# Optimization experiments

Measured on AMD Instinct MI355X. Metric: run time of the kernel, lower is better.

## Reference

```python
import jax, jax.numpy as jnp
import numpy as np

B, T, DM, H, DQ, FF, L, OUT = 4, 512, 768, 8, 32, 3072, 6, 80
D_REL = 100   # relative_positional_distance
NEG = 1e8
LN_EPS = 1e-5


def _layer_norm(x, w, b):
    mu = jnp.mean(x, axis=-1, keepdims=True)
    var = jnp.mean((x - mu) ** 2, axis=-1, keepdims=True)
    return (x - mu) * jax.lax.rsqrt(var + LN_EPS) * w + b


def _attention(x, wq, wk, wv, wo, rel):
    # x: (B,T,DM); wq/wk/wv: (H,DM,DQ); wo: (H,DQ,DM); rel: (H, 2*D_REL-1, DQ)
    Tq = x.shape[1]
    q = jnp.einsum('btf,hfa->bhta', x, wq) / (DQ ** 0.5)   # q pre-scaled (as in source)
    k = jnp.einsum('btf,hfa->bhta', x, wk)
    v = jnp.einsum('btf,hfa->bhta', x, wv)
    logits = jnp.einsum('bhqa,bhka->bhqk', q, k)

    # relative positional logits over the 199 learned offsets
    rel_log = jnp.einsum('bhqd,hmd->bhqm', q, rel)          # (B,H,T,2*D_REL-1)
    pad = Tq - D_REL
    if pad > 0:
        # zero-pad to 2T-1 rel positions, then mask out-of-range offsets with -1e8
        rel_log = jnp.pad(rel_log, ((0, 0), (0, 0), (0, 0), (pad, pad)))
        m = jnp.arange(2 * Tq - 1)
        oob = (m < pad) | (m >= 2 * Tq - 1 - pad)
        rel_log = rel_log - NEG * oob.astype(rel_log.dtype)
    else:
        start = D_REL - Tq
        rel_log = rel_log[..., start:start + 2 * Tq - 1]
    # relative -> absolute indexing: pos[..., i, j] = rel_log[..., i, (j - i) + T - 1]
    idx = jnp.arange(Tq)[None, :] - jnp.arange(Tq)[:, None] + (Tq - 1)   # (T,T)
    pos = jnp.take_along_axis(rel_log, idx[None, None], axis=-1)         # (B,H,T,T)

    probs = jax.nn.softmax(logits + pos, axis=-1)
    o = jnp.einsum('bhqk,bhka->bhqa', probs, v)
    return jnp.einsum('bhta,had->btd', o, wo)


def _forward(x, wq, wk, wv, wo, rel, lin1_w, lin1_b, lin2_w, lin2_b,
             ln1_w, ln1_b, ln2_w, ln2_b, w_out, b_out):
    def step(h, p):
        (q, k, v, o, r, l1w, l1b, l2w, l2b, n1w, n1b, n2w, n2b) = p
        a = _attention(h, q, k, v, o, r)
        h = _layer_norm(h + a, n1w, n1b)                  # post-norm, residual
        ff = jnp.maximum(h @ l1w.T + l1b, 0.0) @ l2w.T + l2b
        h = _layer_norm(h + ff, n2w, n2b)
        return h, None
    h, _ = jax.lax.scan(step, x, (wq, wk, wv, wo, rel, lin1_w, lin1_b,
                                  lin2_w, lin2_b, ln1_w, ln1_b, ln2_w, ln2_b))
    return h @ w_out.T + b_out                            # (B,T,OUT)


def setup_inputs() -> dict:
    key = jax.random.key(0)
    ks = jax.random.split(key, 16)
    n = lambda k, shape, scale: (jax.random.normal(k, shape, dtype=jnp.float32) * scale)
    s_qkv = (2.0 / (DM + DQ)) ** 0.5      # xavier_normal_ scale
    s_o = (2.0 / (DQ + DM)) ** 0.5
    return {
        'x':      n(ks[0], (B, T, DM), 1.0),
        'wq':     n(ks[1], (L, H, DM, DQ), s_qkv),
        'wk':     n(ks[2], (L, H, DM, DQ), s_qkv),
        'wv':     n(ks[3], (L, H, DM, DQ), s_qkv),
        'wo':     n(ks[4], (L, H, DQ, DM), s_o),
        'rel':    n(ks[5], (L, H, 2 * D_REL - 1, DQ), DQ ** -0.5),
        'lin1_w': n(ks[6], (L, FF, DM), DM ** -0.5),
        'lin1_b': jnp.zeros((L, FF), jnp.float32),
        'lin2_w': n(ks[7], (L, DM, FF), FF ** -0.5),
        'lin2_b': jnp.zeros((L, DM), jnp.float32),
        'ln1_w':  jnp.ones((L, DM), jnp.float32),
        'ln1_b':  jnp.zeros((L, DM), jnp.float32),
        'ln2_w':  jnp.ones((L, DM), jnp.float32),
        'ln2_b':  jnp.zeros((L, DM), jnp.float32),
        'w_out':  n(ks[8], (OUT, DM), DM ** -0.5),
        'b_out':  jnp.zeros((OUT,), jnp.float32),
    }


def reference(x, wq, wk, wv, wo, rel, lin1_w, lin1_b, lin2_w, lin2_b,
              ln1_w, ln1_b, ln2_w, ln2_b, w_out, b_out):
    return _forward(x, wq, wk, wv, wo, rel, lin1_w, lin1_b, lin2_w, lin2_b,
                    ln1_w, ln1_b, ln2_w, ln2_b, w_out, b_out)
```

## Files before the change

kernel.cpp:

```cpp
#include <hip/hip_runtime.h>

typedef _Float16 f16;
typedef f16 f16x8 __attribute__((ext_vector_type(8)));
typedef f16 f16x4 __attribute__((ext_vector_type(4)));
typedef float f32x4 __attribute__((ext_vector_type(4)));

#define B_ 4
#define T_ 512
#define DM_ 768
#define H_ 8
#define DQ_ 32
#define FF_ 3072
#define L_ 6
#define OUT_ 80
#define M_ (B_*T_)

__device__ __forceinline__ void gload16(const f16* g, f16* l) {
    __builtin_amdgcn_global_load_lds(
        (const __attribute__((address_space(1))) unsigned int*)g,
        (__attribute__((address_space(3))) unsigned int*)l, 16, 0, 0);
}

template<int N> __device__ __forceinline__ void wait_vm() {
    if constexpr (N == 0)      asm volatile("s_waitcnt vmcnt(0)" ::: "memory");
    else if constexpr (N == 3) asm volatile("s_waitcnt vmcnt(3)" ::: "memory");
    else if constexpr (N == 4) asm volatile("s_waitcnt vmcnt(4)" ::: "memory");
    else if constexpr (N == 6) asm volatile("s_waitcnt vmcnt(6)" ::: "memory");
    else if constexpr (N == 8) asm volatile("s_waitcnt vmcnt(8)" ::: "memory");
    else                       asm volatile("s_waitcnt vmcnt(0)" ::: "memory");
}


#define PKU_X  196608L
#define PKU_L1 (PKU_X + 1769472L)
#define PKU_L2 (PKU_L1 + 1769472L)
#define PKB_VEC 14592
#define PKB_LIN 1632
#define PKB_QKV 1728
#define PKB_WO  1152
#define PKB_TOTAL (PKB_VEC + PKB_LIN + PKB_QKV + PKB_WO)

__global__ void pack_all_kernel(
    const float* __restrict__ x, const float* __restrict__ wq, const float* __restrict__ wk,
    const float* __restrict__ wv, const float* __restrict__ wo, const float* __restrict__ rel,
    const float* __restrict__ lin1w, const float* __restrict__ lin2w, const float* __restrict__ wout,
    f16* __restrict__ xH, f16* __restrict__ BTqkv, f16* __restrict__ BTwo,
    f16* __restrict__ lin1H, f16* __restrict__ lin2H, f16* __restrict__ woutH, f16* __restrict__ relH)
{
    __shared__ float tile[64 * 33];
    const int bid = blockIdx.x, tid = threadIdx.x;
    if (bid < PKB_VEC) {
        const long u = (long)bid * 256 + tid;
        const float* src; f16* dst; long off;
        if (u < PKU_X)       { src = x;     dst = xH;    off = u; }
        else if (u < PKU_L1) { src = lin1w; dst = lin1H; off = u - PKU_X; }
        else                 { src = lin2w; dst = lin2H; off = u - PKU_L1; }
        const float4 v0 = ((const float4*)src)[off * 2];
        const float4 v1 = ((const float4*)src)[off * 2 + 1];
        f16x8 o;
        o[0] = (f16)v0.x; o[1] = (f16)v0.y; o[2] = (f16)v0.z; o[3] = (f16)v0.w;
        o[4] = (f16)v1.x; o[5] = (f16)v1.y; o[6] = (f16)v1.z; o[7] = (f16)v1.w;
        ((f16x8*)dst)[off] = o;
    } else if (bid < PKB_VEC + PKB_LIN) {
        const long u = (long)(bid - PKB_VEC) * 256 + tid;
        if (u < 98304) {
            const int k = (int)(u % 768), n = (int)(u / 768);
            woutH[u] = (n < OUT_) ? (f16)wout[n * 768 + k] : (f16)0;
        } else {
            const long v2 = u - 98304;
            const int a = (int)(v2 & 31);
            const long t = v2 >> 5;
            const int d = (int)(t % 208);
            const int lh = (int)(t / 208);
            relH[v2] = (d < 199) ? (f16)rel[((long)lh * 199 + d) * 32 + a] : (f16)0;
        }
    } else if (bid < PKB_VEC + PKB_LIN + PKB_QKV) {
        const int g = bid - (PKB_VEC + PKB_LIN);
        const int kb = g % 12;
        const int grp = g / 12;
        const int h = grp & 7, sec = (grp >> 3) % 3, l = grp / 24;
        const float* w = (sec == 0) ? wq : (sec == 1 ? wk : wv);
        const float* src = w + (((long)l * 8 + h) * 768 + kb * 64) * 32;
        const float scale = (sec == 0) ? 0.17677669529663687f : 1.f;
#pragma unroll
        for (int p = 0; p < 2; ++p) {
            const int kk = p * 32 + (tid >> 3), a = (tid & 7) * 4;
            const float4 v = *(const float4*)(src + (long)kk * 32 + a);
            tile[kk * 33 + a]     = v.x * scale;
            tile[kk * 33 + a + 1] = v.y * scale;
            tile[kk * 33 + a + 2] = v.z * scale;
            tile[kk * 33 + a + 3] = v.w * scale;
        }
        __syncthreads();
        f16* dst = BTqkv + ((long)l * 768 + sec * 256 + h * 32) * 768 + kb * 64;
        {
            const int a = tid >> 3, k8 = (tid & 7) * 8;
            f16x8 o;
#pragma unroll
            for (int e = 0; e < 8; ++e) o[e] = (f16)tile[(k8 + e) * 33 + a];
            *(f16x8*)(dst + (long)a * 768 + k8) = o;
        }
    } else {
        const int g = bid - (PKB_VEC + PKB_LIN + PKB_QKV);
        const int nb = g % 24;
        const int tmp = g / 24;
        const int kb2 = tmp % 8, l = tmp / 8;
        const float* src = wo + ((long)l * 256 + kb2 * 32) * 768 + nb * 32;
        {
            const int r = tid >> 3, c = (tid & 7) * 4;
            const float4 v = *(const float4*)(src + (long)r * 768 + c);
            tile[r * 33 + c]     = v.x;
            tile[r * 33 + c + 1] = v.y;
            tile[r * 33 + c + 2] = v.z;
            tile[r * 33 + c + 3] = v.w;
        }
        __syncthreads();
        if (tid < 128) {
            const int n = tid >> 2, k8 = (tid & 3) * 8;
            f16x8 o;
#pragma unroll
            for (int e = 0; e < 8; ++e) o[e] = (f16)tile[(k8 + e) * 33 + n];
            f16* dst = BTwo + ((long)l * 768 + nb * 32 + n) * 256 + kb2 * 32 + k8;
            *(f16x8*)dst = o;
        }
    }
}

__device__ __forceinline__ void xcd_tile(int BM, int BN, int& m0, int& n0) {
    const int gx = gridDim.x;
    const int id = blockIdx.y * gx + blockIdx.x;
    const int cpx = (gx * gridDim.y) >> 3;
    const int t = (id & 7) * cpx + (id >> 3);
    m0 = (t / gx) * BM;
    n0 = (t % gx) * BN;
}


template<int BM, int BN>
__global__ __launch_bounds__(256) void gemm7_kernel(
    const f16* __restrict__ A, const f16* __restrict__ Bt,
    const float* __restrict__ bias, const float* __restrict__ res,
    float* __restrict__ outF, f16* __restrict__ outH, f16* __restrict__ vTout,
    int M, int N, int K, int mode, int ldOut, int nMax)
{
    constexpr int IA = BM / 32;
    constexpr int JF = BN / 32;
    constexpr int LA = BM / 32;
    constexpr int LB = BN / 32;
    constexpr int L  = LA + LB;
    __shared__ __align__(16) f16 As[2][BM * 64];
    __shared__ __align__(16) f16 Bs[2][BN * 64];
    const int tid = threadIdx.x;
    const int wave = tid >> 6, lane = tid & 63;
    int m0, n0; xcd_tile(BM, BN, m0, n0);
    const int z = blockIdx.z;
    const int Kl = K / (int)gridDim.z;
    const int kb = z * Kl;
    const int nt = Kl / 64;
    const int wr = wave >> 1, wc = wave & 1;
    const int l15 = lane & 15, l4 = lane >> 4;
    const int lrow = lane >> 3;
    const int lcol = ((lane & 7) ^ (lane >> 3)) * 8;

    const f16* Abase = A  + (long)(m0 + lrow) * K + kb + lcol;
    const f16* Bbase = Bt + (long)(n0 + lrow) * K + kb + lcol;

    f32x4 acc[IA][JF];
#pragma unroll
    for (int i = 0; i < IA; ++i)
#pragma unroll
        for (int j = 0; j < JF; ++j) acc[i][j] = (f32x4){0.f, 0.f, 0.f, 0.f};

    auto stage = [&](int buf, int k0) {
#pragma unroll
        for (int i = 0; i < LA; ++i) {
            const int c = wave + 4 * i;
            gload16(Abase + (long)c * 8 * K + k0, &As[buf][c * 512]);
        }
#pragma unroll
        for (int i = 0; i < LB; ++i) {
            const int c = wave + 4 * i;
            gload16(Bbase + (long)c * 8 * K + k0, &Bs[buf][c * 512]);
        }
    };

    stage(0, 0);
    int cur = 0;
    for (int t = 0; t < nt; ++t) {
        if (t + 1 < nt) { stage(cur ^ 1, (t + 1) * 64); wait_vm<L>(); }
        else            { wait_vm<0>(); }
        __builtin_amdgcn_s_barrier();
#pragma unroll
        for (int s = 0; s < 2; ++s) {
            f16x8 af[IA], bf[JF];
#pragma unroll
            for (int i = 0; i < IA; ++i) {
                const int row = wr * (BM / 2) + i * 16 + l15;
                af[i] = *(const f16x8*)&As[cur][row * 64 + (((s * 4 + l4) ^ (l15 & 7)) * 8)];
            }
#pragma unroll
            for (int j = 0; j < JF; ++j) {
                const int row = wc * (BN / 2) + j * 16 + l15;
                bf[j] = *(const f16x8*)&Bs[cur][row * 64 + (((s * 4 + l4) ^ (l15 & 7)) * 8)];
            }
#pragma unroll
            for (int i = 0; i < IA; ++i)
#pragma unroll
                for (int j = 0; j < JF; ++j)
                    acc[i][j] = __builtin_amdgcn_mfma_f32_16x16x32_f16(af[i], bf[j], acc[i][j], 0, 0, 0);
        }
        __builtin_amdgcn_s_barrier();
        cur ^= 1;
    }

#pragma unroll
    for (int i = 0; i < IA; ++i) {
#pragma unroll
        for (int j = 0; j < JF; ++j) {
            const int col = n0 + wc * (BN / 2) + j * 16 + l15;
            if (mode & 32) {
#pragma unroll
                for (int r = 0; r < 4; ++r) {
                    const int row = m0 + wr * (BM / 2) + i * 16 + l4 * 4 + r;
                    float v = acc[i][j][r];
                    if (col < 512) {
                        outH[(long)row * 512 + col] = (f16)v;
                    } else {
                        const int bb = row >> 9, t = row & 511;
                        vTout[((long)(bb * 256 + (col - 512))) * 512 + t] = (f16)v;
                    }
                }
            } else if (mode & 64) {
                float* po = outF + (long)z * M * ldOut;
#pragma unroll
                for (int r = 0; r < 4; ++r) {
                    const int row = m0 + wr * (BM / 2) + i * 16 + l4 * 4 + r;
                    po[(long)row * ldOut + col] = acc[i][j][r];
                }
            } else if (col < nMax) {
                const float bvv = (mode & 1) ? bias[col] : 0.f;
#pragma unroll
                for (int r = 0; r < 4; ++r) {
                    const int row = m0 + wr * (BM / 2) + i * 16 + l4 * 4 + r;
                    float v = acc[i][j][r] + bvv;
                    if (mode & 2) v += res[(long)row * N + col];
                    if (mode & 4) v = fmaxf(v, 0.f);
                    if (mode & 8)  outF[(long)row * ldOut + col] = v;
                    if (mode & 16) outH[(long)row * ldOut + col] = (f16)v;
                }
            }
        }
    }
}


__global__ __launch_bounds__(256) void attn_kernel(
    const f16* __restrict__ qkvH, const f16* __restrict__ vT,
    const f16* __restrict__ relH, int l, f16* __restrict__ o)
{
    __shared__ __align__(16) f16 Qs[64 * 40];
    __shared__ __align__(16) f16 Ks[288 * 40];
    __shared__ __align__(16) f16 Vt[32 * 296];
    __shared__ __align__(16) f16 Ps[64 * 296];
    __shared__ __align__(16) f16 Rl[64 * 216];
    const int tid = threadIdx.x;
    const int qb = blockIdx.x, h = blockIdx.y, b = blockIdx.z;
    const int q0 = qb * 64;
    int lo = q0 - 99; lo = (lo > 0) ? (lo & ~7) : 0;
    const int hi = min(512, q0 + 163);
    const int nk = hi - lo;

    {
        const int r = tid >> 2, c = tid & 3;
        *(f16x8*)&Qs[r * 40 + c * 8] =
            *(const f16x8*)(qkvH + ((long)(b * 512 + q0 + r)) * 512 + h * 32 + c * 8);
    }
    for (int idx = tid; idx < 288 * 4; idx += 256) {
        const int r = idx >> 2, c = idx & 3;
        f16x8 v = {};
        if (r < nk)
            v = *(const f16x8*)(qkvH + ((long)(b * 512 + lo + r)) * 512 + 256 + h * 32 + c * 8);
        *(f16x8*)&Ks[r * 40 + c * 8] = v;
    }
    for (int idx = tid; idx < 32 * 36; idx += 256) {
        const int a = idx / 36, k8 = idx % 36;
        f16x8 v = {};
        const int kbase = k8 * 8;
        if (kbase < nk) {
            const f16* src = vT + ((long)(b * 256 + h * 32 + a)) * 512 + lo + kbase;
            if (kbase + 8 <= nk) {
                v = *(const f16x8*)src;
            } else {
#pragma unroll
                for (int e = 0; e < 8; ++e) if (kbase + e < nk) v[e] = src[e];
            }
        }
        *(f16x8*)&Vt[a * 296 + kbase] = v;
    }
    __syncthreads();

    const int wave = tid >> 6, lane = tid & 63;
    const int l15 = lane & 15, l4 = lane >> 4;
    const int qloc = wave * 16;

    const f16x8 qf = *(const f16x8*)&Qs[(qloc + l15) * 40 + l4 * 8];

    const f16* relh = relH + ((long)(l * 8 + h)) * 208 * 32;
    {
        f32x4 racc[13];
#pragma unroll
        for (int fd = 0; fd < 13; ++fd) {
            const f16x8 bf = *(const f16x8*)(relh + (fd * 16 + l15) * 32 + l4 * 8);
            racc[fd] = __builtin_amdgcn_mfma_f32_16x16x32_f16(qf, bf, (f32x4){0.f,0.f,0.f,0.f}, 0, 0, 0);
        }
#pragma unroll
        for (int fd = 0; fd < 13; ++fd)
#pragma unroll
            for (int r = 0; r < 4; ++r)
                Rl[(qloc + l4 * 4 + r) * 216 + fd * 16 + l15] = (f16)racc[fd][r];
    }

    f32x4 sacc[18];
#pragma unroll
    for (int fk = 0; fk < 18; ++fk) {
        const f16x8 bf = *(const f16x8*)&Ks[(fk * 16 + l15) * 40 + l4 * 8];
        sacc[fk] = __builtin_amdgcn_mfma_f32_16x16x32_f16(qf, bf, (f32x4){0.f,0.f,0.f,0.f}, 0, 0, 0);
    }

    float mx[4] = {-1e30f, -1e30f, -1e30f, -1e30f};
#pragma unroll
    for (int fk = 0; fk < 18; ++fk) {
        const int kk = fk * 16 + l15;
        const int k = lo + kk;
#pragma unroll
        for (int r = 0; r < 4; ++r) {
            const int q = q0 + qloc + l4 * 4 + r;
            const int d = k - q + 99;
            float v = -1e30f;
            if (kk < nk && d >= 0 && d < 199)
                v = sacc[fk][r] + (float)Rl[(qloc + l4 * 4 + r) * 216 + d];
            sacc[fk][r] = v;
            mx[r] = fmaxf(mx[r], v);
        }
    }
#pragma unroll
    for (int r = 0; r < 4; ++r) {
        mx[r] = fmaxf(mx[r], __shfl_xor(mx[r], 1));
        mx[r] = fmaxf(mx[r], __shfl_xor(mx[r], 2));
        mx[r] = fmaxf(mx[r], __shfl_xor(mx[r], 4));
        mx[r] = fmaxf(mx[r], __shfl_xor(mx[r], 8));
    }
    float sum[4] = {0.f, 0.f, 0.f, 0.f};
#pragma unroll
    for (int fk = 0; fk < 18; ++fk) {
        const int kk = fk * 16 + l15;
#pragma unroll
        for (int r = 0; r < 4; ++r) {
            const float p = __expf(sacc[fk][r] - mx[r]);
            sum[r] += p;
            Ps[(qloc + l4 * 4 + r) * 296 + kk] = (f16)p;
        }
    }
#pragma unroll
    for (int r = 0; r < 4; ++r) {
        sum[r] += __shfl_xor(sum[r], 1);
        sum[r] += __shfl_xor(sum[r], 2);
        sum[r] += __shfl_xor(sum[r], 4);
        sum[r] += __shfl_xor(sum[r], 8);
    }

    f32x4 oacc[2] = {{0.f,0.f,0.f,0.f}, {0.f,0.f,0.f,0.f}};
#pragma unroll
    for (int ks = 0; ks < 9; ++ks) {
        const f16x8 pa = *(const f16x8*)&Ps[(qloc + l15) * 296 + ks * 32 + l4 * 8];
#pragma unroll
        for (int j = 0; j < 2; ++j) {
            const f16x8 vb = *(const f16x8*)&Vt[(j * 16 + l15) * 296 + ks * 32 + l4 * 8];
            oacc[j] = __builtin_amdgcn_mfma_f32_16x16x32_f16(pa, vb, oacc[j], 0, 0, 0);
        }
    }

    f16* ob = o + ((long)(b * 512 + q0 + qloc + l4 * 4)) * 256 + h * 32;
#pragma unroll
    for (int r = 0; r < 4; ++r) {
        const float inv = 1.f / sum[r];
#pragma unroll
        for (int j = 0; j < 2; ++j)
            ob[(long)r * 256 + j * 16 + l15] = (f16)(oacc[j][r] * inv);
    }
}


__global__ __launch_bounds__(256) void ln_kernel(
    const float* __restrict__ src, const float* __restrict__ w, const float* __restrict__ bb,
    float* __restrict__ outF, f16* __restrict__ outH)
{
    __shared__ float red1[4], red2[4];
    const int row = blockIdx.x, tid = threadIdx.x;
    const float* x = src + (long)row * 768;
    float v0 = x[tid], v1 = x[tid + 256], v2 = x[tid + 512];
    float s = v0 + v1 + v2;
#pragma unroll
    for (int off = 32; off > 0; off >>= 1) s += __shfl_xor(s, off);
    if ((tid & 63) == 0) red1[tid >> 6] = s;
    __syncthreads();
    const float mu = (red1[0] + red1[1] + red1[2] + red1[3]) * (1.f / 768.f);
    const float d0 = v0 - mu, d1 = v1 - mu, d2 = v2 - mu;
    float ss = d0 * d0 + d1 * d1 + d2 * d2;
#pragma unroll
    for (int off = 32; off > 0; off >>= 1) ss += __shfl_xor(ss, off);
    if ((tid & 63) == 0) red2[tid >> 6] = ss;
    __syncthreads();
    const float var = (red2[0] + red2[1] + red2[2] + red2[3]) * (1.f / 768.f);
    const float inv = rsqrtf(var + 1e-5f);
    float y0 = d0 * inv * w[tid]       + bb[tid];
    float y1 = d1 * inv * w[tid + 256] + bb[tid + 256];
    float y2 = d2 * inv * w[tid + 512] + bb[tid + 512];
    long base = (long)row * 768;
    outF[base + tid] = y0; outF[base + tid + 256] = y1; outF[base + tid + 512] = y2;
    outH[base + tid] = (f16)y0; outH[base + tid + 256] = (f16)y1; outH[base + tid + 512] = (f16)y2;
}


__global__ __launch_bounds__(256) void ln_sum4_kernel(
    const float* __restrict__ p,
    const float* __restrict__ bias, const float* __restrict__ res,
    const float* __restrict__ w, const float* __restrict__ bb,
    float* __restrict__ outF, f16* __restrict__ outH)
{
    __shared__ float red1[4], red2[4];
    const int row = blockIdx.x, tid = threadIdx.x;
    const long rb = (long)row * 768;
    float v[3];
#pragma unroll
    for (int i = 0; i < 3; ++i) {
        const int c = tid + i * 256;
        float s = bias[c] + res[rb + c];
#pragma unroll
        for (int zz = 0; zz < 4; ++zz) s += p[((long)zz * M_ + row) * 768 + c];
        v[i] = s;
    }
    float s = v[0] + v[1] + v[2];
#pragma unroll
    for (int off = 32; off > 0; off >>= 1) s += __shfl_xor(s, off);
    if ((tid & 63) == 0) red1[tid >> 6] = s;
    __syncthreads();
    const float mu = (red1[0] + red1[1] + red1[2] + red1[3]) * (1.f / 768.f);
    const float d0 = v[0] - mu, d1 = v[1] - mu, d2 = v[2] - mu;
    float ss = d0 * d0 + d1 * d1 + d2 * d2;
#pragma unroll
    for (int off = 32; off > 0; off >>= 1) ss += __shfl_xor(ss, off);
    if ((tid & 63) == 0) red2[tid >> 6] = ss;
    __syncthreads();
    const float var = (red2[0] + red2[1] + red2[2] + red2[3]) * (1.f / 768.f);
    const float inv = rsqrtf(var + 1e-5f);
    float y0 = d0 * inv * w[tid]       + bb[tid];
    float y1 = d1 * inv * w[tid + 256] + bb[tid + 256];
    float y2 = d2 * inv * w[tid + 512] + bb[tid + 512];
    outF[rb + tid] = y0; outF[rb + tid + 256] = y1; outF[rb + tid + 512] = y2;
    outH[rb + tid] = (f16)y0; outH[rb + tid + 256] = (f16)y1; outH[rb + tid + 512] = (f16)y2;
}


extern "C" void kernel_launch(void* const* d_in, const int* in_sizes, int n_in,
                              void* d_out, int out_size, void* d_ws, size_t ws_size,
                              hipStream_t stream) {
    const float* x     = (const float*)d_in[0];
    const float* wq    = (const float*)d_in[1];
    const float* wk    = (const float*)d_in[2];
    const float* wv    = (const float*)d_in[3];
    const float* wo    = (const float*)d_in[4];
    const float* rel   = (const float*)d_in[5];
    const float* lin1w = (const float*)d_in[6];
    const float* lin1b = (const float*)d_in[7];
    const float* lin2w = (const float*)d_in[8];
    const float* lin2b = (const float*)d_in[9];
    const float* ln1w  = (const float*)d_in[10];
    const float* ln1b  = (const float*)d_in[11];
    const float* ln2w  = (const float*)d_in[12];
    const float* ln2b  = (const float*)d_in[13];
    const float* wout  = (const float*)d_in[14];
    const float* bout  = (const float*)d_in[15];

    char* base = (char*)d_ws;
    size_t off = 0;
    auto alloc = [&](size_t bytes) {
        void* p = base + off;
        off = (off + bytes + 255) & ~(size_t)255;
        return p;
    };
    f16*   xH    = (f16*)  alloc((size_t)M_ * 768 * 2);
    f16*   BTqkv = (f16*)  alloc((size_t)L_ * 768 * 768 * 2);
    f16*   BTwo  = (f16*)  alloc((size_t)L_ * 768 * 256 * 2);
    f16*   lin1H = (f16*)  alloc((size_t)L_ * 3072 * 768 * 2);
    f16*   lin2H = (f16*)  alloc((size_t)L_ * 768 * 3072 * 2);
    f16*   woutH = (f16*)  alloc((size_t)128 * 768 * 2);
    f16*   relH  = (f16*)  alloc((size_t)L_ * 8 * 208 * 32 * 2);
    f16*   qkvH  = (f16*)  alloc((size_t)M_ * 512 * 2);
    f16*   vTbuf = (f16*)  alloc((size_t)B_ * 256 * 512 * 2);
    float* scrF  = (float*)alloc((size_t)M_ * 768 * 4);
    float* part  = (float*)alloc((size_t)4 * M_ * 768 * 4);
    f16*   oH    = (f16*)  alloc((size_t)M_ * 256 * 2);
    float* ln1F  = (float*)alloc((size_t)M_ * 768 * 4);
    f16*   ln1H  = (f16*)  alloc((size_t)M_ * 768 * 2);
    f16*   ffH   = (f16*)  alloc((size_t)M_ * 3072 * 2);
    float* hF    = (float*)alloc((size_t)M_ * 768 * 4);
    f16*   hH    = (f16*)  alloc((size_t)M_ * 768 * 2);
    (void)ws_size; (void)in_sizes; (void)n_in; (void)out_size;

    pack_all_kernel<<<PKB_TOTAL, 256, 0, stream>>>(
        x, wq, wk, wv, wo, rel, lin1w, lin2w, wout,
        xH, BTqkv, BTwo, lin1H, lin2H, woutH, relH);

    for (int l = 0; l < L_; ++l) {
        const f16*   aIn   = (l == 0) ? xH : hH;
        const float* resIn = (l == 0) ? x  : hF;
        gemm7_kernel<32, 64><<<dim3(12, 64, 1), 256, 0, stream>>>(
            aIn, BTqkv + (size_t)l * 768 * 768, nullptr, nullptr, nullptr, qkvH, vTbuf,
            M_, 768, 768, 32, 512, 768);
        attn_kernel<<<dim3(8, 8, 4), 256, 0, stream>>>(qkvH, vTbuf, relH, l, oH);
        gemm7_kernel<32, 64><<<dim3(12, 64, 1), 256, 0, stream>>>(
            oH, BTwo + (size_t)l * 768 * 256, nullptr, resIn, scrF, nullptr, nullptr,
            M_, 768, 256, 2 | 8, 768, 768);
        ln_kernel<<<M_, 256, 0, stream>>>(scrF, ln1w + l * 768, ln1b + l * 768, ln1F, ln1H);
        gemm7_kernel<128, 64><<<dim3(48, 16, 1), 256, 0, stream>>>(
            ln1H, lin1H + (size_t)l * 3072 * 768, lin1b + l * 3072, nullptr, nullptr, ffH, nullptr,
            M_, 3072, 768, 1 | 4 | 16, 3072, 3072);
        gemm7_kernel<128, 64><<<dim3(12, 16, 4), 256, 0, stream>>>(
            ffH, lin2H + (size_t)l * 768 * 3072, nullptr, nullptr, part, nullptr, nullptr,
            M_, 768, 3072, 64, 768, 768);
        ln_sum4_kernel<<<M_, 256, 0, stream>>>(part, lin2b + l * 768, ln1F,
                                               ln2w + l * 768, ln2b + l * 768, hF, hH);
    }
    gemm7_kernel<32, 64><<<dim3(2, 64, 1), 256, 0, stream>>>(
        hH, woutH, bout, nullptr, (float*)d_out, nullptr, nullptr,
        M_, 80, 768, 1 | 8, 80, 80);
}
```

Measured before the change: 512.7 us.

## Shrink attention LDS by aliasing scratch buffers and loading Q directly

The attention kernel reuses one shared buffer for the relative-position logits and the probability tile, since each wave only touches its own rows. It also drops the Q staging buffer in favour of direct global loads, and trims the key tile from 288 to 272 rows. The barrier moves after the relative-logit MFMAs so that work overlaps with the K/V loads. The pack kernel now converts 16 floats per thread on half as many blocks. The aim is lower LDS use per block, so more blocks fit per CU, plus less launch overhead in packing. The risk is subtle aliasing or padding errors in the shared scratch.

```diff
diff --git a/kernel.cpp b/kernel.cpp
--- a/kernel.cpp
+++ b/kernel.cpp
@@ -26,15 +26,14 @@
     else if constexpr (N == 3) asm volatile("s_waitcnt vmcnt(3)" ::: "memory");
     else if constexpr (N == 4) asm volatile("s_waitcnt vmcnt(4)" ::: "memory");
     else if constexpr (N == 6) asm volatile("s_waitcnt vmcnt(6)" ::: "memory");
-    else if constexpr (N == 8) asm volatile("s_waitcnt vmcnt(8)" ::: "memory");
     else                       asm volatile("s_waitcnt vmcnt(0)" ::: "memory");
 }
 
 
-#define PKU_X  196608L
-#define PKU_L1 (PKU_X + 1769472L)
-#define PKU_L2 (PKU_L1 + 1769472L)
-#define PKB_VEC 14592
+#define PKU_X  98304L
+#define PKU_L1 (PKU_X + 884736L)
+#define PKU_L2 (PKU_L1 + 884736L)
+#define PKB_VEC 7296
 #define PKB_LIN 1632
 #define PKB_QKV 1728
 #define PKB_WO  1152
@@ -55,12 +54,17 @@
         if (u < PKU_X)       { src = x;     dst = xH;    off = u; }
         else if (u < PKU_L1) { src = lin1w; dst = lin1H; off = u - PKU_X; }
         else                 { src = lin2w; dst = lin2H; off = u - PKU_L1; }
-        const float4 v0 = ((const float4*)src)[off * 2];
-        const float4 v1 = ((const float4*)src)[off * 2 + 1];
-        f16x8 o;
-        o[0] = (f16)v0.x; o[1] = (f16)v0.y; o[2] = (f16)v0.z; o[3] = (f16)v0.w;
-        o[4] = (f16)v1.x; o[5] = (f16)v1.y; o[6] = (f16)v1.z; o[7] = (f16)v1.w;
-        ((f16x8*)dst)[off] = o;
+        const float4 v0 = ((const float4*)src)[off * 4];
+        const float4 v1 = ((const float4*)src)[off * 4 + 1];
+        const float4 v2 = ((const float4*)src)[off * 4 + 2];
+        const float4 v3 = ((const float4*)src)[off * 4 + 3];
+        f16x8 o0, o1;
+        o0[0] = (f16)v0.x; o0[1] = (f16)v0.y; o0[2] = (f16)v0.z; o0[3] = (f16)v0.w;
+        o0[4] = (f16)v1.x; o0[5] = (f16)v1.y; o0[6] = (f16)v1.z; o0[7] = (f16)v1.w;
+        o1[0] = (f16)v2.x; o1[1] = (f16)v2.y; o1[2] = (f16)v2.z; o1[3] = (f16)v2.w;
+        o1[4] = (f16)v3.x; o1[5] = (f16)v3.y; o1[6] = (f16)v3.z; o1[7] = (f16)v3.w;
+        ((f16x8*)dst)[off * 2]     = o0;
+        ((f16x8*)dst)[off * 2 + 1] = o1;
     } else if (bid < PKB_VEC + PKB_LIN) {
         const long u = (long)(bid - PKB_VEC) * 256 + tid;
         if (u < 98304) {
@@ -258,11 +262,9 @@
     const f16* __restrict__ qkvH, const f16* __restrict__ vT,
     const f16* __restrict__ relH, int l, f16* __restrict__ o)
 {
-    __shared__ __align__(16) f16 Qs[64 * 40];
-    __shared__ __align__(16) f16 Ks[288 * 40];
+    __shared__ __align__(16) f16 Ks[272 * 40];
     __shared__ __align__(16) f16 Vt[32 * 296];
-    __shared__ __align__(16) f16 Ps[64 * 296];
-    __shared__ __align__(16) f16 Rl[64 * 216];
+    __shared__ __align__(16) f16 Scr[64 * 296];
     const int tid = threadIdx.x;
     const int qb = blockIdx.x, h = blockIdx.y, b = blockIdx.z;
     const int q0 = qb * 64;
@@ -270,12 +272,7 @@
     const int hi = min(512, q0 + 163);
     const int nk = hi - lo;
 
-    {
-        const int r = tid >> 2, c = tid & 3;
-        *(f16x8*)&Qs[r * 40 + c * 8] =
-            *(const f16x8*)(qkvH + ((long)(b * 512 + q0 + r)) * 512 + h * 32 + c * 8);
-    }
-    for (int idx = tid; idx < 288 * 4; idx += 256) {
+    for (int idx = tid; idx < 272 * 4; idx += 256) {
         const int r = idx >> 2, c = idx & 3;
         f16x8 v = {};
         if (r < nk)
@@ -297,13 +294,12 @@
         }
         *(f16x8*)&Vt[a * 296 + kbase] = v;
     }
-    __syncthreads();
 
     const int wave = tid >> 6, lane = tid & 63;
     const int l15 = lane & 15, l4 = lane >> 4;
     const int qloc = wave * 16;
 
-    const f16x8 qf = *(const f16x8*)&Qs[(qloc + l15) * 40 + l4 * 8];
+    const f16x8 qf = *(const f16x8*)(qkvH + ((long)(b * 512 + q0 + qloc + l15)) * 512 + h * 32 + l4 * 8);
 
     const f16* relh = relH + ((long)(l * 8 + h)) * 208 * 32;
     {
@@ -317,19 +313,20 @@
         for (int fd = 0; fd < 13; ++fd)
 #pragma unroll
             for (int r = 0; r < 4; ++r)
-                Rl[(qloc + l4 * 4 + r) * 216 + fd * 16 + l15] = (f16)racc[fd][r];
-    }
-
-    f32x4 sacc[18];
-#pragma unroll
-    for (int fk = 0; fk < 18; ++fk) {
+                Scr[(qloc + l4 * 4 + r) * 296 + fd * 16 + l15] = (f16)racc[fd][r];
+    }
+    __syncthreads();
+
+    f32x4 sacc[17];
+#pragma unroll
+    for (int fk = 0; fk < 17; ++fk) {
         const f16x8 bf = *(const f16x8*)&Ks[(fk * 16 + l15) * 40 + l4 * 8];
         sacc[fk] = __builtin_amdgcn_mfma_f32_16x16x32_f16(qf, bf, (f32x4){0.f,0.f,0.f,0.f}, 0, 0, 0);
     }
 
     float mx[4] = {-1e30f, -1e30f, -1e30f, -1e30f};
 #pragma unroll
-    for (int fk = 0; fk < 18; ++fk) {
+    for (int fk = 0; fk < 17; ++fk) {
         const int kk = fk * 16 + l15;
         const int k = lo + kk;
 #pragma unroll
@@ -338,7 +335,7 @@
             const int d = k - q + 99;
             float v = -1e30f;
             if (kk < nk && d >= 0 && d < 199)
-                v = sacc[fk][r] + (float)Rl[(qloc + l4 * 4 + r) * 216 + d];
+                v = sacc[fk][r] + (float)Scr[(qloc + l4 * 4 + r) * 296 + d];
             sacc[fk][r] = v;
             mx[r] = fmaxf(mx[r], v);
         }
@@ -352,15 +349,18 @@
     }
     float sum[4] = {0.f, 0.f, 0.f, 0.f};
 #pragma unroll
-    for (int fk = 0; fk < 18; ++fk) {
+    for (int fk = 0; fk < 17; ++fk) {
         const int kk = fk * 16 + l15;
 #pragma unroll
         for (int r = 0; r < 4; ++r) {
             const float p = __expf(sacc[fk][r] - mx[r]);
             sum[r] += p;
-            Ps[(qloc + l4 * 4 + r) * 296 + kk] = (f16)p;
-        }
-    }
+            Scr[(qloc + l4 * 4 + r) * 296 + kk] = (f16)p;
+        }
+    }
+#pragma unroll
+    for (int r = 0; r < 4; ++r)
+        Scr[(qloc + l4 * 4 + r) * 296 + 272 + l15] = (f16)0;
 #pragma unroll
     for (int r = 0; r < 4; ++r) {
         sum[r] += __shfl_xor(sum[r], 1);
@@ -372,7 +372,7 @@
     f32x4 oacc[2] = {{0.f,0.f,0.f,0.f}, {0.f,0.f,0.f,0.f}};
 #pragma unroll
     for (int ks = 0; ks < 9; ++ks) {
-        const f16x8 pa = *(const f16x8*)&Ps[(qloc + l15) * 296 + ks * 32 + l4 * 8];
+        const f16x8 pa = *(const f16x8*)&Scr[(qloc + l15) * 296 + ks * 32 + l4 * 8];
 #pragma unroll
         for (int j = 0; j < 2; ++j) {
             const f16x8 vb = *(const f16x8*)&Vt[(j * 16 + l15) * 296 + ks * 32 + l4 * 8];
```

Measured after the change: 512.2 us. No clear change (-0.1%).
